# Optimization experiments

Measured on AMD Instinct MI355X. Metric: run time of the kernel, lower is better.

Reference implementation:

```python
import jax, jax.numpy as jnp
import numpy as np

B, T, D, H, L, V = 16, 1024, 512, 8, 6, 96
HS = D // H
FF = 4 * D


def setup_inputs() -> dict:
    key = jax.random.key(0)
    ks = jax.random.split(key, 16)
    n = lambda k, shape: jax.random.normal(k, shape, jnp.float32) * 0.02
    return {
        "idx": jax.random.randint(ks[0], (B, T), 0, V),
        "targets": jax.random.randint(ks[1], (B, T), 0, V),
        "tok_emb": n(ks[2], (V, D)),
        "pos_emb": n(ks[3], (T, D)),
        "Wq": n(ks[4], (L, H, D, HS)),
        "Wk": n(ks[5], (L, H, D, HS)),
        "Wv": n(ks[6], (L, H, D, HS)),
        "Wproj": n(ks[7], (L, D, D)),
        "bproj": jnp.zeros((L, D), jnp.float32),
        "W1": n(ks[8], (L, D, FF)),
        "b1": jnp.zeros((L, FF), jnp.float32),
        "W2": n(ks[9], (L, FF, D)),
        "b2": jnp.zeros((L, D), jnp.float32),
        "ln1_s": jnp.ones((L, D), jnp.float32),
        "ln1_b": jnp.zeros((L, D), jnp.float32),
        "ln2_s": jnp.ones((L, D), jnp.float32),
        "ln2_b": jnp.zeros((L, D), jnp.float32),
        "lnf_s": jnp.ones((D,), jnp.float32),
        "lnf_b": jnp.zeros((D,), jnp.float32),
        "Wout": n(ks[10], (D, V)),
        "bout": jnp.zeros((V,), jnp.float32),
    }


def _ln(x, s, b, eps=1e-5):
    m = x.mean(-1, keepdims=True)
    v = ((x - m) ** 2).mean(-1, keepdims=True)
    return (x - m) * jax.lax.rsqrt(v + eps) * s + b


def reference(idx, targets, tok_emb, pos_emb, Wq, Wk, Wv, Wproj, bproj,
              W1, b1, W2, b2, ln1_s, ln1_b, ln2_s, ln2_b, lnf_s, lnf_b,
              Wout, bout):
    x = tok_emb[idx] + pos_emb[:T]  # [B,T,D]
    causal = jnp.tril(jnp.ones((T, T), jnp.bool_))
    scale = D ** (-0.5)  # NOTE: source scales by full channel dim, not head_size
    for l in range(L):
        h = _ln(x, ln1_s[l], ln1_b[l])
        q = jnp.einsum("btd,hdk->bhtk", h, Wq[l])
        k = jnp.einsum("btd,hdk->bhtk", h, Wk[l])
        v = jnp.einsum("btd,hdk->bhtk", h, Wv[l])
        att = jnp.einsum("bhtk,bhsk->bhts", q, k) * scale
        att = jnp.where(causal, att, -jnp.inf)
        att = jax.nn.softmax(att, axis=-1)
        o = jnp.einsum("bhts,bhsk->bhtk", att, v)
        o = o.transpose(0, 2, 1, 3).reshape(B, T, D)  # concat heads
        x = x + (o @ Wproj[l] + bproj[l])
        h2 = _ln(x, ln2_s[l], ln2_b[l])
        x = x + (jnp.maximum(h2 @ W1[l] + b1[l], 0.0) @ W2[l] + b2[l])
    x = _ln(x, lnf_s, lnf_b)
    logits = (x @ Wout + bout).reshape(B * T, V)
    logp = jax.nn.log_softmax(logits, axis=-1)
    loss = -logp[jnp.arange(B * T), targets.reshape(-1)].mean()
    return logits, loss
```

## Files before the change

### kernel.cpp

```cpp
#include <hip/hip_runtime.h>

#define B_  16
#define T_  1024
#define D_  512
#define H_  8
#define L_  6
#define V_  96
#define HS_ 64
#define FF_ 2048
#define BT_ (B_*T_)

typedef __attribute__((ext_vector_type(8))) short bf16x8;
typedef __attribute__((ext_vector_type(4))) float f32x4;

typedef __attribute__((address_space(3))) unsigned int lds_u32_t;
typedef const __attribute__((address_space(1))) unsigned int glb_u32_t;

__device__ __forceinline__ void gload16(const unsigned short* g, unsigned short* l) {
  __builtin_amdgcn_global_load_lds((glb_u32_t*)g, (lds_u32_t*)l, 16, 0, 0);
}

__device__ __forceinline__ unsigned short f2b(float f) {
  unsigned u = __float_as_uint(f);
  unsigned r = (u + 0x7FFFu + ((u >> 16) & 1u)) >> 16;
  return (unsigned short)r;
}

__global__ void zero_kernel(float* p) { p[0] = 0.f; }

__global__ __launch_bounds__(128) void embed_kernel(const int* __restrict__ idx,
    const float* __restrict__ tok, const float* __restrict__ pos, float* __restrict__ x) {
  int bt = blockIdx.x;
  int t  = bt & (T_ - 1);
  int id = idx[bt];
  if (id < 0) id = 0; if (id > V_ - 1) id = V_ - 1;
  int d  = threadIdx.x * 4;
  float4 tv = *(const float4*)(tok + (size_t)id * D_ + d);
  float4 pv = *(const float4*)(pos + (size_t)t  * D_ + d);
  float4 o = {tv.x + pv.x, tv.y + pv.y, tv.z + pv.z, tv.w + pv.w};
  *(float4*)(x + (size_t)bt * D_ + d) = o;
}

__global__ __launch_bounds__(256) void transpose_cvt(const float* __restrict__ src,
    unsigned short* __restrict__ dst, int R, int C, long sstride, long dstride) {
  __shared__ float t[32][33];
  const float* s = src + (size_t)blockIdx.z * sstride;
  unsigned short* d = dst + (size_t)blockIdx.z * dstride;
  int r0 = blockIdx.y * 32, c0 = blockIdx.x * 32;
  int tr = threadIdx.x >> 5, tc = threadIdx.x & 31;
#pragma unroll
  for (int i = 0; i < 4; ++i)
    t[tr + i * 8][tc] = s[(size_t)(r0 + tr + i * 8) * C + c0 + tc];
  __syncthreads();
#pragma unroll
  for (int i = 0; i < 4; ++i)
    d[(size_t)(c0 + tr + i * 8) * R + r0 + tc] = f2b(t[tc][tr + i * 8]);
}

template<bool BF16OUT>
__global__ __launch_bounds__(256) void ln_kernel(const float* __restrict__ x,
    const float* __restrict__ s, const float* __restrict__ b, void* __restrict__ outv) {
  int wave = threadIdx.x >> 6;
  int lane = threadIdx.x & 63;
  int r = blockIdx.x * 4 + wave;
  const float* xr = x + (size_t)r * D_;
  float vals[8];
  float sum = 0.f;
#pragma unroll
  for (int j = 0; j < 8; ++j) { vals[j] = xr[j * 64 + lane]; sum += vals[j]; }
#pragma unroll
  for (int o = 32; o > 0; o >>= 1) sum += __shfl_xor(sum, o, 64);
  float mean = sum * (1.f / D_);
  float vs = 0.f;
#pragma unroll
  for (int j = 0; j < 8; ++j) { float d = vals[j] - mean; vs += d * d; }
#pragma unroll
  for (int o = 32; o > 0; o >>= 1) vs += __shfl_xor(vs, o, 64);
  float rstd = rsqrtf(vs * (1.f / D_) + 1e-5f);
#pragma unroll
  for (int j = 0; j < 8; ++j) {
    int c = j * 64 + lane;
    float v = (vals[j] - mean) * rstd * s[c] + b[c];
    if (BF16OUT) ((unsigned short*)outv)[(size_t)r * D_ + c] = f2b(v);
    else         ((float*)outv)[(size_t)r * D_ + c] = v;
  }
}

#define BK 32
template<bool ACC, bool RELU, bool BIAS, int OUTMODE>
__global__ __launch_bounds__(256) void mfma_gemm(
    const unsigned short* __restrict__ A,
    const unsigned short* __restrict__ Bt,
    const float* __restrict__ bias,
    void* __restrict__ Cv,
    int K, int ldc) {
  __shared__ unsigned short Al[128 * BK];
  __shared__ unsigned short Bl[128 * BK];
  const int m0 = blockIdx.x * 128, n0 = blockIdx.y * 128;
  const int tid = threadIdx.x;
  const int lane = tid & 63, wave = tid >> 6;
  const int wy = wave >> 1, wx = wave & 1;
  const int l15 = lane & 15, quad = lane >> 4;

  const int sbase = wave * 1024;
  const int soff  = sbase + lane * 16;
  const int r0 = soff >> 6, c0e = (soff & 63) >> 1;
  const int r1 = r0 + 64;
  const unsigned short* gA0 = A  + (size_t)(m0 + r0) * K + c0e;
  const unsigned short* gA1 = A  + (size_t)(m0 + r1) * K + c0e;
  const unsigned short* gB0 = Bt + (size_t)(n0 + r0) * K + c0e;
  const unsigned short* gB1 = Bt + (size_t)(n0 + r1) * K + c0e;
  unsigned short* lA0 = &Al[sbase >> 1];
  unsigned short* lA1 = &Al[(sbase + 4096) >> 1];
  unsigned short* lB0 = &Bl[sbase >> 1];
  unsigned short* lB1 = &Bl[(sbase + 4096) >> 1];

  f32x4 acc[4][4];
  const f32x4 z4 = {0.f, 0.f, 0.f, 0.f};
#pragma unroll
  for (int mi = 0; mi < 4; ++mi)
#pragma unroll
    for (int ni = 0; ni < 4; ++ni) acc[mi][ni] = z4;

  for (int k0 = 0; k0 < K; k0 += BK) {
    gload16(gA0 + k0, lA0);
    gload16(gA1 + k0, lA1);
    gload16(gB0 + k0, lB0);
    gload16(gB1 + k0, lB1);
    __syncthreads();
    bf16x8 af[4], bfr[4];
#pragma unroll
    for (int mi = 0; mi < 4; ++mi)
      af[mi] = *(const bf16x8*)(&Al[(wy * 64 + mi * 16 + l15) * BK + quad * 8]);
#pragma unroll
    for (int ni = 0; ni < 4; ++ni)
      bfr[ni] = *(const bf16x8*)(&Bl[(wx * 64 + ni * 16 + l15) * BK + quad * 8]);
#pragma unroll
    for (int mi = 0; mi < 4; ++mi)
#pragma unroll
      for (int ni = 0; ni < 4; ++ni)
        acc[mi][ni] = __builtin_amdgcn_mfma_f32_16x16x32_bf16(af[mi], bfr[ni], acc[mi][ni], 0, 0, 0);
    __syncthreads();
  }
#pragma unroll
  for (int mi = 0; mi < 4; ++mi) {
    int row0 = m0 + wy * 64 + mi * 16 + quad * 4;
#pragma unroll
    for (int ni = 0; ni < 4; ++ni) {
      int col = n0 + wx * 64 + ni * 16 + l15;
      float bb = BIAS ? bias[col] : 0.f;
#pragma unroll
      for (int r = 0; r < 4; ++r) {
        float v = acc[mi][ni][r] + bb;
        if (RELU) v = fmaxf(v, 0.f);
        int row = row0 + r;
        if (OUTMODE == 2) {
          int b = row >> 10, t = row & (T_ - 1);
          int h = col >> 6, hs = col & 63;
          ((unsigned short*)Cv)[((size_t)((b * H_ + h) * HS_ + hs)) * T_ + t] = f2b(v);
        } else {
          size_t off = (size_t)row * ldc + col;
          if (ACC) v += ((const float*)Cv)[off];
          if (OUTMODE == 1) ((unsigned short*)Cv)[off] = f2b(v);
          else              ((float*)Cv)[off] = v;
        }
      }
    }
  }
}

#define PSTR 72
__global__ __launch_bounds__(256) void attn_mfma(const unsigned short* __restrict__ q,
    const unsigned short* __restrict__ k, const unsigned short* __restrict__ vt,
    unsigned short* __restrict__ o) {
  __shared__ unsigned short Pbuf[2][64 * PSTR];
  __shared__ float Lsum[4][64];
  const int qt = (gridDim.x - 1) - blockIdx.x;
  const int bh = blockIdx.y;
  const int b = bh >> 3, hh = bh & 7;
  const int tid = threadIdx.x;
  const int lane = tid & 63, w = tid >> 6;
  const int l15 = lane & 15, quad = lane >> 4;
  const float CEXP = 0.044194173824159216f * 1.4426950408889634f;

  bf16x8 qf[4][2];
#pragma unroll
  for (int mi = 0; mi < 4; ++mi)
#pragma unroll
    for (int c = 0; c < 2; ++c)
      qf[mi][c] = *(const bf16x8*)(q + (size_t)(b * T_ + qt * 64 + mi * 16 + l15) * D_
                                     + hh * HS_ + c * 32 + quad * 8);

  f32x4 oacc[4];
  float psum[4][4];
  const f32x4 z4 = {0.f, 0.f, 0.f, 0.f};
#pragma unroll
  for (int mi = 0; mi < 4; ++mi) {
    oacc[mi] = z4;
#pragma unroll
    for (int r = 0; r < 4; ++r) psum[mi][r] = 0.f;
  }

  const unsigned short* kbase = k  + (size_t)(b * T_ + w * 16 + l15) * D_ + hh * HS_ + quad * 8;
  const unsigned short* vbase = vt + ((size_t)(bh * HS_ + w * 16 + l15)) * T_ + quad * 8;

  bf16x8 kf[2], vf[2];
#pragma unroll
  for (int c = 0; c < 2; ++c) {
    kf[c] = *(const bf16x8*)(kbase + c * 32);
    vf[c] = *(const bf16x8*)(vbase + c * 32);
  }

  const int gc = w * 16 + l15;

  for (int kt = 0; kt <= qt; ++kt) {
    const int ktn = (kt < qt) ? kt + 1 : qt;
    bf16x8 kfn[2], vfn[2];
#pragma unroll
    for (int c = 0; c < 2; ++c) {
      kfn[c] = *(const bf16x8*)(kbase + (size_t)ktn * 64 * D_ + c * 32);
      vfn[c] = *(const bf16x8*)(vbase + ktn * 64 + c * 32);
    }

    f32x4 s[4];
#pragma unroll
    for (int mi = 0; mi < 4; ++mi) s[mi] = z4;
    __builtin_amdgcn_s_setprio(1);
#pragma unroll
    for (int c = 0; c < 2; ++c)
#pragma unroll
      for (int mi = 0; mi < 4; ++mi)
        s[mi] = __builtin_amdgcn_mfma_f32_16x16x32_bf16(qf[mi][c], kf[c], s[mi], 0, 0, 0);
    __builtin_amdgcn_s_setprio(0);

    unsigned short* pb = Pbuf[kt & 1];
    if (kt == qt) {
#pragma unroll
      for (int mi = 0; mi < 4; ++mi)
#pragma unroll
        for (int r = 0; r < 4; ++r) {
          int row = mi * 16 + quad * 4 + r;
          float p = (gc > row) ? 0.f : exp2f(s[mi][r] * CEXP);
          unsigned short us = f2b(p);
          psum[mi][r] += __uint_as_float((unsigned)us << 16);
          pb[row * PSTR + gc] = us;
        }
    } else {
#pragma unroll
      for (int mi = 0; mi < 4; ++mi)
#pragma unroll
        for (int r = 0; r < 4; ++r) {
          int row = mi * 16 + quad * 4 + r;
          float p = exp2f(s[mi][r] * CEXP);
          unsigned short us = f2b(p);
          psum[mi][r] += __uint_as_float((unsigned)us << 16);
          pb[row * PSTR + gc] = us;
        }
    }
    __syncthreads();
    __builtin_amdgcn_s_setprio(1);
#pragma unroll
    for (int c = 0; c < 2; ++c) {
#pragma unroll
      for (int mi = 0; mi < 4; ++mi) {
        bf16x8 pf = *(const bf16x8*)(&pb[(mi * 16 + l15) * PSTR + c * 32 + quad * 8]);
        oacc[mi] = __builtin_amdgcn_mfma_f32_16x16x32_bf16(pf, vf[c], oacc[mi], 0, 0, 0);
      }
    }
    __builtin_amdgcn_s_setprio(0);
#pragma unroll
    for (int c = 0; c < 2; ++c) { kf[c] = kfn[c]; vf[c] = vfn[c]; }
  }

#pragma unroll
  for (int mi = 0; mi < 4; ++mi)
#pragma unroll
    for (int r = 0; r < 4; ++r) {
#pragma unroll
      for (int off = 1; off < 16; off <<= 1)
        psum[mi][r] += __shfl_xor(psum[mi][r], off, 64);
    }
  if (l15 == 0) {
#pragma unroll
    for (int mi = 0; mi < 4; ++mi)
#pragma unroll
      for (int r = 0; r < 4; ++r)
        Lsum[w][mi * 16 + quad * 4 + r] = psum[mi][r];
  }
  __syncthreads();
#pragma unroll
  for (int mi = 0; mi < 4; ++mi)
#pragma unroll
    for (int r = 0; r < 4; ++r) {
      int row = mi * 16 + quad * 4 + r;
      float inv = 1.f / (Lsum[0][row] + Lsum[1][row] + Lsum[2][row] + Lsum[3][row]);
      o[(size_t)(b * T_ + qt * 64 + row) * D_ + hh * HS_ + w * 16 + l15] =
          f2b(oacc[mi][r] * inv);
    }
}

__global__ __launch_bounds__(256) void gemm_f32_kernel(const float* __restrict__ A, int lda,
    const float* __restrict__ Bw, int ldb, const float* __restrict__ bias,
    float* __restrict__ C, int ldc, int K, int N) {
  __shared__ float As[16][64];
  __shared__ float Bs[16][64];
  int n0 = blockIdx.y * 64;
  int nv = N - n0; if (nv > 64) nv = 64;
  int m0 = blockIdx.x * 64;
  const int tid = threadIdx.x;
  const int tx = tid & 15, ty = tid >> 4;
  const int amm = tid >> 2;
  const int akk = (tid & 3) * 4;
  const int bkk = tid >> 4;
  const int bnn = (tid & 15) * 4;
  float acc[4][4] = {};
  for (int k0 = 0; k0 < K; k0 += 16) {
    float4 av = *(const float4*)(A + (size_t)(m0 + amm) * lda + k0 + akk);
    As[akk + 0][amm] = av.x; As[akk + 1][amm] = av.y;
    As[akk + 2][amm] = av.z; As[akk + 3][amm] = av.w;
    if (bnn < nv) {
      float4 bv = *(const float4*)(Bw + (size_t)(k0 + bkk) * ldb + n0 + bnn);
      Bs[bkk][bnn + 0] = bv.x; Bs[bkk][bnn + 1] = bv.y;
      Bs[bkk][bnn + 2] = bv.z; Bs[bkk][bnn + 3] = bv.w;
    } else {
      Bs[bkk][bnn + 0] = 0.f; Bs[bkk][bnn + 1] = 0.f;
      Bs[bkk][bnn + 2] = 0.f; Bs[bkk][bnn + 3] = 0.f;
    }
    __syncthreads();
#pragma unroll
    for (int kk = 0; kk < 16; ++kk) {
      float4 a4 = *(const float4*)(&As[kk][ty * 4]);
      float4 b4 = *(const float4*)(&Bs[kk][tx * 4]);
      float aa[4] = {a4.x, a4.y, a4.z, a4.w};
      float bb[4] = {b4.x, b4.y, b4.z, b4.w};
#pragma unroll
      for (int i = 0; i < 4; ++i)
#pragma unroll
        for (int j = 0; j < 4; ++j)
          acc[i][j] = fmaf(aa[i], bb[j], acc[i][j]);
    }
    __syncthreads();
  }
  if (tx * 4 < nv) {
#pragma unroll
    for (int i = 0; i < 4; ++i) {
      float* cp = C + (size_t)(m0 + ty * 4 + i) * ldc + n0 + tx * 4;
      float4 st = {acc[i][0] + bias[n0 + tx * 4 + 0], acc[i][1] + bias[n0 + tx * 4 + 1],
                   acc[i][2] + bias[n0 + tx * 4 + 2], acc[i][3] + bias[n0 + tx * 4 + 3]};
      *(float4*)cp = st;
    }
  }
}

__global__ __launch_bounds__(256) void loss_kernel(const float* __restrict__ logits,
    const int* __restrict__ targets, float* __restrict__ loss_acc) {
  __shared__ float wsum[4];
  int wave = threadIdx.x >> 6, lane = threadIdx.x & 63;
  float local = 0.f;
  for (int r = blockIdx.x * 4 + wave; r < BT_; r += gridDim.x * 4) {
    const float* lr = logits + (size_t)r * V_;
    float v0 = lr[lane];
    float v1 = (lane < 32) ? lr[64 + lane] : -INFINITY;
    float mx = fmaxf(v0, v1);
#pragma unroll
    for (int o = 32; o > 0; o >>= 1) mx = fmaxf(mx, __shfl_xor(mx, o, 64));
    float se = expf(v0 - mx) + ((lane < 32) ? expf(v1 - mx) : 0.f);
#pragma unroll
    for (int o = 32; o > 0; o >>= 1) se += __shfl_xor(se, o, 64);
    if (lane == 0) {
      int tg = targets[r];
      if (tg < 0) tg = 0; if (tg > V_ - 1) tg = V_ - 1;
      local += (mx + logf(se)) - lr[tg];
    }
  }
  if (lane == 0) wsum[wave] = local;
  __syncthreads();
  if (threadIdx.x == 0)
    atomicAdd(loss_acc, wsum[0] + wsum[1] + wsum[2] + wsum[3]);
}

__global__ void loss_finalize_kernel(const float* __restrict__ acc, float* __restrict__ out) {
  out[(size_t)BT_ * V_] = acc[0] * (1.f / BT_);
}

static void* g_ws_fallback = nullptr;

extern "C" void kernel_launch(void* const* d_in, const int* in_sizes, int n_in,
                              void* d_out, int out_size, void* d_ws, size_t ws_size,
                              hipStream_t stream) {
  const int*   idx     = (const int*)d_in[0];
  const int*   targets = (const int*)d_in[1];
  const float* tok  = (const float*)d_in[2];
  const float* pos  = (const float*)d_in[3];
  const float* Wq   = (const float*)d_in[4];
  const float* Wk   = (const float*)d_in[5];
  const float* Wv   = (const float*)d_in[6];
  const float* Wp   = (const float*)d_in[7];
  const float* bp   = (const float*)d_in[8];
  const float* W1   = (const float*)d_in[9];
  const float* b1   = (const float*)d_in[10];
  const float* W2   = (const float*)d_in[11];
  const float* b2   = (const float*)d_in[12];
  const float* l1s  = (const float*)d_in[13];
  const float* l1b  = (const float*)d_in[14];
  const float* l2s  = (const float*)d_in[15];
  const float* l2b  = (const float*)d_in[16];
  const float* lfs  = (const float*)d_in[17];
  const float* lfb  = (const float*)d_in[18];
  const float* Wout = (const float*)d_in[19];
  const float* bout = (const float*)d_in[20];
  float* out = (float*)d_out;

  const size_t n_x  = (size_t)BT_ * D_;
  const size_t n_wT = 9437184;
  const size_t need_floats = n_x + n_x + n_x / 2 + n_x / 2 + n_x / 2 +
                             (size_t)BT_ * FF_ / 2 + n_wT + 256;
  const size_t need_bytes  = need_floats * sizeof(float);

  float* ws;
  if (ws_size >= need_bytes) {
    ws = (float*)d_ws;
  } else {
    if (!g_ws_fallback) (void)hipMalloc(&g_ws_fallback, need_bytes);
    ws = (float*)g_ws_fallback;
  }

  size_t off = 0;
  float* x  = ws + off; off += n_x;
  float* qf32 = ws + off; off += n_x;
  unsigned short* qb = (unsigned short*)qf32;
  unsigned short* kb  = (unsigned short*)(ws + off); off += n_x / 2;
  unsigned short* vtb = (unsigned short*)(ws + off); off += n_x / 2;
  unsigned short* hb  = (unsigned short*)(ws + off); off += n_x / 2;
  unsigned short* ffb = (unsigned short*)(ws + off); off += (size_t)BT_ * FF_ / 2;
  unsigned short* wqT = (unsigned short*)(ws + off);
  unsigned short* wkT = wqT + (size_t)L_ * D_ * D_;
  unsigned short* wvT = wkT + (size_t)L_ * D_ * D_;
  unsigned short* wpT = wvT + (size_t)L_ * D_ * D_;
  unsigned short* w1T = wpT + (size_t)L_ * D_ * D_;
  unsigned short* w2T = w1T + (size_t)L_ * D_ * FF_;
  off += n_wT;
  float* lacc = ws + off;

  zero_kernel<<<1, 1, 0, stream>>>(lacc);
  embed_kernel<<<BT_, 128, 0, stream>>>(idx, tok, pos, x);

  transpose_cvt<<<dim3(2, 16, 48), 256, 0, stream>>>(Wq, wqT, 512, 64, 32768, 32768);
  transpose_cvt<<<dim3(2, 16, 48), 256, 0, stream>>>(Wk, wkT, 512, 64, 32768, 32768);
  transpose_cvt<<<dim3(2, 16, 48), 256, 0, stream>>>(Wv, wvT, 512, 64, 32768, 32768);
  transpose_cvt<<<dim3(16, 16, 6), 256, 0, stream>>>(Wp, wpT, 512, 512, 262144, 262144);
  transpose_cvt<<<dim3(64, 16, 6), 256, 0, stream>>>(W1, w1T, 512, 2048, 1048576, 1048576);
  transpose_cvt<<<dim3(16, 64, 6), 256, 0, stream>>>(W2, w2T, 2048, 512, 1048576, 1048576);

  const dim3 gD(BT_ / 128, D_ / 128);
  const dim3 gF(BT_ / 128, FF_ / 128);

  for (int l = 0; l < L_; ++l) {
    ln_kernel<true><<<BT_ / 4, 256, 0, stream>>>(x, l1s + (size_t)l * D_, l1b + (size_t)l * D_, hb);
    mfma_gemm<false, false, false, 1><<<gD, 256, 0, stream>>>(
        hb, wqT + (size_t)l * D_ * D_, nullptr, qb, D_, D_);
    mfma_gemm<false, false, false, 1><<<gD, 256, 0, stream>>>(
        hb, wkT + (size_t)l * D_ * D_, nullptr, kb, D_, D_);
    mfma_gemm<false, false, false, 2><<<gD, 256, 0, stream>>>(
        hb, wvT + (size_t)l * D_ * D_, nullptr, vtb, D_, D_);
    attn_mfma<<<dim3(T_ / 64, B_ * H_), 256, 0, stream>>>(qb, kb, vtb, hb);
    mfma_gemm<true, false, true, 0><<<gD, 256, 0, stream>>>(
        hb, wpT + (size_t)l * D_ * D_, bp + (size_t)l * D_, x, D_, D_);
    ln_kernel<true><<<BT_ / 4, 256, 0, stream>>>(x, l2s + (size_t)l * D_, l2b + (size_t)l * D_, hb);
    mfma_gemm<false, true, true, 1><<<gF, 256, 0, stream>>>(
        hb, w1T + (size_t)l * D_ * FF_, b1 + (size_t)l * FF_, ffb, D_, FF_);
    mfma_gemm<true, false, true, 0><<<gD, 256, 0, stream>>>(
        ffb, w2T + (size_t)l * FF_ * D_, b2 + (size_t)l * D_, x, FF_, D_);
  }

  ln_kernel<false><<<BT_ / 4, 256, 0, stream>>>(x, lfs, lfb, qf32);
  gemm_f32_kernel<<<dim3(BT_ / 64, 2), 256, 0, stream>>>(
      qf32, D_, Wout, V_, bout, out, V_, D_, V_);
  loss_kernel<<<64, 256, 0, stream>>>(out, targets, lacc);
  loss_finalize_kernel<<<1, 1, 0, stream>>>(lacc, out);
}
```

Baseline: 2.136 ms.

## Fuse QKV projections into one GEMM and double-buffer GEMM LDS tiles

Concatenates the transposed Wq/Wk/Wv weights per layer so a single GEMM with 12 column tiles writes Q and K into an interleaved row-major buffer of stride 1024 and V into the transposed layout. Attention is updated to read Q/K with the new stride. Separately, the MFMA GEMM now double-buffers its LDS tiles, issuing the next K-step's global-to-LDS loads before computing the current one and using one barrier per step instead of two. This aims to cut launch count, re-reads of the normalized activations, and load stalls, at the cost of twice the LDS per block, which may lower occupancy.

Measured after the change: 2.065 ms. 1.03x faster.

```diff
diff --git a/kernel.cpp b/kernel.cpp
--- a/kernel.cpp
+++ b/kernel.cpp
@@ -9,6 +9,7 @@
 #define HS_ 64
 #define FF_ 2048
 #define BT_ (B_*T_)
+#define QKS 1024
 
 typedef __attribute__((ext_vector_type(8))) short bf16x8;
 typedef __attribute__((ext_vector_type(4))) float f32x4;
@@ -42,10 +43,12 @@
 }
 
 __global__ __launch_bounds__(256) void transpose_cvt(const float* __restrict__ src,
-    unsigned short* __restrict__ dst, int R, int C, long sstride, long dstride) {
+    unsigned short* __restrict__ dst, int R, int C, long sstride, long dstride,
+    int zper, long zouter) {
   __shared__ float t[32][33];
   const float* s = src + (size_t)blockIdx.z * sstride;
-  unsigned short* d = dst + (size_t)blockIdx.z * dstride;
+  unsigned short* d = dst + (size_t)(blockIdx.z / zper) * zouter
+                          + (size_t)(blockIdx.z % zper) * dstride;
   int r0 = blockIdx.y * 32, c0 = blockIdx.x * 32;
   int tr = threadIdx.x >> 5, tc = threadIdx.x & 31;
 #pragma unroll
@@ -92,10 +95,10 @@
     const unsigned short* __restrict__ A,
     const unsigned short* __restrict__ Bt,
     const float* __restrict__ bias,
-    void* __restrict__ Cv,
+    void* __restrict__ Cv, void* __restrict__ Cv2,
     int K, int ldc) {
-  __shared__ unsigned short Al[128 * BK];
-  __shared__ unsigned short Bl[128 * BK];
+  __shared__ unsigned short Al[2][128 * BK];
+  __shared__ unsigned short Bl[2][128 * BK];
   const int m0 = blockIdx.x * 128, n0 = blockIdx.y * 128;
   const int tid = threadIdx.x;
   const int lane = tid & 63, wave = tid >> 6;
@@ -106,14 +109,11 @@
   const int soff  = sbase + lane * 16;
   const int r0 = soff >> 6, c0e = (soff & 63) >> 1;
   const int r1 = r0 + 64;
+  const int ls = sbase >> 1;
   const unsigned short* gA0 = A  + (size_t)(m0 + r0) * K + c0e;
   const unsigned short* gA1 = A  + (size_t)(m0 + r1) * K + c0e;
   const unsigned short* gB0 = Bt + (size_t)(n0 + r0) * K + c0e;
   const unsigned short* gB1 = Bt + (size_t)(n0 + r1) * K + c0e;
-  unsigned short* lA0 = &Al[sbase >> 1];
-  unsigned short* lA1 = &Al[(sbase + 4096) >> 1];
-  unsigned short* lB0 = &Bl[sbase >> 1];
-  unsigned short* lB1 = &Bl[(sbase + 4096) >> 1];
 
   f32x4 acc[4][4];
   const f32x4 z4 = {0.f, 0.f, 0.f, 0.f};
@@ -122,26 +122,40 @@
 #pragma unroll
     for (int ni = 0; ni < 4; ++ni) acc[mi][ni] = z4;
 
-  for (int k0 = 0; k0 < K; k0 += BK) {
-    gload16(gA0 + k0, lA0);
-    gload16(gA1 + k0, lA1);
-    gload16(gB0 + k0, lB0);
-    gload16(gB1 + k0, lB1);
-    __syncthreads();
+  gload16(gA0, &Al[0][ls]);
+  gload16(gA1, &Al[0][ls + 2048]);
+  gload16(gB0, &Bl[0][ls]);
+  gload16(gB1, &Bl[0][ls + 2048]);
+  __syncthreads();
+
+  const int nsteps = K / BK;
+  int cur = 0;
+  for (int s = 0; s < nsteps; ++s) {
+    if (s + 1 < nsteps) {
+      const int k0 = (s + 1) * BK;
+      gload16(gA0 + k0, &Al[cur ^ 1][ls]);
+      gload16(gA1 + k0, &Al[cur ^ 1][ls + 2048]);
+      gload16(gB0 + k0, &Bl[cur ^ 1][ls]);
+      gload16(gB1 + k0, &Bl[cur ^ 1][ls + 2048]);
+    }
     bf16x8 af[4], bfr[4];
 #pragma unroll
     for (int mi = 0; mi < 4; ++mi)
-      af[mi] = *(const bf16x8*)(&Al[(wy * 64 + mi * 16 + l15) * BK + quad * 8]);
+      af[mi] = *(const bf16x8*)(&Al[cur][(wy * 64 + mi * 16 + l15) * BK + quad * 8]);
 #pragma unroll
     for (int ni = 0; ni < 4; ++ni)
-      bfr[ni] = *(const bf16x8*)(&Bl[(wx * 64 + ni * 16 + l15) * BK + quad * 8]);
+      bfr[ni] = *(const bf16x8*)(&Bl[cur][(wx * 64 + ni * 16 + l15) * BK + quad * 8]);
 #pragma unroll
     for (int mi = 0; mi < 4; ++mi)
 #pragma unroll
       for (int ni = 0; ni < 4; ++ni)
         acc[mi][ni] = __builtin_amdgcn_mfma_f32_16x16x32_bf16(af[mi], bfr[ni], acc[mi][ni], 0, 0, 0);
-    __syncthreads();
-  }
+    if (s + 1 < nsteps) {
+      __syncthreads();
+      cur ^= 1;
+    }
+  }
+
 #pragma unroll
   for (int mi = 0; mi < 4; ++mi) {
     int row0 = m0 + wy * 64 + mi * 16 + quad * 4;
@@ -154,10 +168,15 @@
         float v = acc[mi][ni][r] + bb;
         if (RELU) v = fmaxf(v, 0.f);
         int row = row0 + r;
-        if (OUTMODE == 2) {
-          int b = row >> 10, t = row & (T_ - 1);
-          int h = col >> 6, hs = col & 63;
-          ((unsigned short*)Cv)[((size_t)((b * H_ + h) * HS_ + hs)) * T_ + t] = f2b(v);
+        if (OUTMODE == 3) {
+          if (col < 1024) {
+            ((unsigned short*)Cv)[(size_t)row * QKS + col] = f2b(v);
+          } else {
+            int vcol = col - 1024;
+            int b = row >> 10, t = row & (T_ - 1);
+            int h = vcol >> 6, hs = vcol & 63;
+            ((unsigned short*)Cv2)[((size_t)((b * H_ + h) * HS_ + hs)) * T_ + t] = f2b(v);
+          }
         } else {
           size_t off = (size_t)row * ldc + col;
           if (ACC) v += ((const float*)Cv)[off];
@@ -188,7 +207,7 @@
   for (int mi = 0; mi < 4; ++mi)
 #pragma unroll
     for (int c = 0; c < 2; ++c)
-      qf[mi][c] = *(const bf16x8*)(q + (size_t)(b * T_ + qt * 64 + mi * 16 + l15) * D_
+      qf[mi][c] = *(const bf16x8*)(q + (size_t)(b * T_ + qt * 64 + mi * 16 + l15) * QKS
                                      + hh * HS_ + c * 32 + quad * 8);
 
   f32x4 oacc[4];
@@ -201,7 +220,7 @@
     for (int r = 0; r < 4; ++r) psum[mi][r] = 0.f;
   }
 
-  const unsigned short* kbase = k  + (size_t)(b * T_ + w * 16 + l15) * D_ + hh * HS_ + quad * 8;
+  const unsigned short* kbase = k  + (size_t)(b * T_ + w * 16 + l15) * QKS + hh * HS_ + quad * 8;
   const unsigned short* vbase = vt + ((size_t)(bh * HS_ + w * 16 + l15)) * T_ + quad * 8;
 
   bf16x8 kf[2], vf[2];
@@ -218,7 +237,7 @@
     bf16x8 kfn[2], vfn[2];
 #pragma unroll
     for (int c = 0; c < 2; ++c) {
-      kfn[c] = *(const bf16x8*)(kbase + (size_t)ktn * 64 * D_ + c * 32);
+      kfn[c] = *(const bf16x8*)(kbase + (size_t)ktn * 64 * QKS + c * 32);
       vfn[c] = *(const bf16x8*)(vbase + ktn * 64 + c * 32);
     }
 
@@ -428,49 +447,48 @@
   size_t off = 0;
   float* x  = ws + off; off += n_x;
   float* qf32 = ws + off; off += n_x;
-  unsigned short* qb = (unsigned short*)qf32;
-  unsigned short* kb  = (unsigned short*)(ws + off); off += n_x / 2;
+  unsigned short* qkb = (unsigned short*)qf32;
+  unsigned short* spare = (unsigned short*)(ws + off); off += n_x / 2;
   unsigned short* vtb = (unsigned short*)(ws + off); off += n_x / 2;
   unsigned short* hb  = (unsigned short*)(ws + off); off += n_x / 2;
   unsigned short* ffb = (unsigned short*)(ws + off); off += (size_t)BT_ * FF_ / 2;
-  unsigned short* wqT = (unsigned short*)(ws + off);
-  unsigned short* wkT = wqT + (size_t)L_ * D_ * D_;
-  unsigned short* wvT = wkT + (size_t)L_ * D_ * D_;
-  unsigned short* wpT = wvT + (size_t)L_ * D_ * D_;
+  unsigned short* wqkvT = (unsigned short*)(ws + off);
+  unsigned short* wpT = wqkvT + (size_t)L_ * 3 * D_ * D_;
   unsigned short* w1T = wpT + (size_t)L_ * D_ * D_;
   unsigned short* w2T = w1T + (size_t)L_ * D_ * FF_;
   off += n_wT;
   float* lacc = ws + off;
+  (void)spare;
+
+  const long DD = (long)D_ * D_;
+  const long L3DD = 3 * DD;
 
   zero_kernel<<<1, 1, 0, stream>>>(lacc);
   embed_kernel<<<BT_, 128, 0, stream>>>(idx, tok, pos, x);
 
-  transpose_cvt<<<dim3(2, 16, 48), 256, 0, stream>>>(Wq, wqT, 512, 64, 32768, 32768);
-  transpose_cvt<<<dim3(2, 16, 48), 256, 0, stream>>>(Wk, wkT, 512, 64, 32768, 32768);
-  transpose_cvt<<<dim3(2, 16, 48), 256, 0, stream>>>(Wv, wvT, 512, 64, 32768, 32768);
-  transpose_cvt<<<dim3(16, 16, 6), 256, 0, stream>>>(Wp, wpT, 512, 512, 262144, 262144);
-  transpose_cvt<<<dim3(64, 16, 6), 256, 0, stream>>>(W1, w1T, 512, 2048, 1048576, 1048576);
-  transpose_cvt<<<dim3(16, 64, 6), 256, 0, stream>>>(W2, w2T, 2048, 512, 1048576, 1048576);
-
+  transpose_cvt<<<dim3(2, 16, 48), 256, 0, stream>>>(Wq, wqkvT,            512, 64, 32768, 32768, 8, L3DD);
+  transpose_cvt<<<dim3(2, 16, 48), 256, 0, stream>>>(Wk, wqkvT + DD,       512, 64, 32768, 32768, 8, L3DD);
+  transpose_cvt<<<dim3(2, 16, 48), 256, 0, stream>>>(Wv, wqkvT + 2 * DD,   512, 64, 32768, 32768, 8, L3DD);
+  transpose_cvt<<<dim3(16, 16, 6), 256, 0, stream>>>(Wp, wpT, 512, 512, 262144, 0, 1, 262144);
+  transpose_cvt<<<dim3(64, 16, 6), 256, 0, stream>>>(W1, w1T, 512, 2048, 1048576, 0, 1, 1048576);
+  transpose_cvt<<<dim3(16, 64, 6), 256, 0, stream>>>(W2, w2T, 2048, 512, 1048576, 0, 1, 1048576);
+
+  const dim3 gQKV(BT_ / 128, 12);
   const dim3 gD(BT_ / 128, D_ / 128);
   const dim3 gF(BT_ / 128, FF_ / 128);
 
   for (int l = 0; l < L_; ++l) {
     ln_kernel<true><<<BT_ / 4, 256, 0, stream>>>(x, l1s + (size_t)l * D_, l1b + (size_t)l * D_, hb);
-    mfma_gemm<false, false, false, 1><<<gD, 256, 0, stream>>>(
-        hb, wqT + (size_t)l * D_ * D_, nullptr, qb, D_, D_);
-    mfma_gemm<false, false, false, 1><<<gD, 256, 0, stream>>>(
-        hb, wkT + (size_t)l * D_ * D_, nullptr, kb, D_, D_);
-    mfma_gemm<false, false, false, 2><<<gD, 256, 0, stream>>>(
-        hb, wvT + (size_t)l * D_ * D_, nullptr, vtb, D_, D_);
-    attn_mfma<<<dim3(T_ / 64, B_ * H_), 256, 0, stream>>>(qb, kb, vtb, hb);
+    mfma_gemm<false, false, false, 3><<<gQKV, 256, 0, stream>>>(
+        hb, wqkvT + (size_t)l * L3DD, nullptr, qkb, vtb, D_, 0);
+    attn_mfma<<<dim3(T_ / 64, B_ * H_), 256, 0, stream>>>(qkb, qkb + 512, vtb, hb);
     mfma_gemm<true, false, true, 0><<<gD, 256, 0, stream>>>(
-        hb, wpT + (size_t)l * D_ * D_, bp + (size_t)l * D_, x, D_, D_);
+        hb, wpT + (size_t)l * DD, bp + (size_t)l * D_, x, nullptr, D_, D_);
     ln_kernel<true><<<BT_ / 4, 256, 0, stream>>>(x, l2s + (size_t)l * D_, l2b + (size_t)l * D_, hb);
     mfma_gemm<false, true, true, 1><<<gF, 256, 0, stream>>>(
-        hb, w1T + (size_t)l * D_ * FF_, b1 + (size_t)l * FF_, ffb, D_, FF_);
+        hb, w1T + (size_t)l * D_ * FF_, b1 + (size_t)l * FF_, ffb, nullptr, D_, FF_);
     mfma_gemm<true, false, true, 0><<<gD, 256, 0, stream>>>(
-        ffb, w2T + (size_t)l * FF_ * D_, b2 + (size_t)l * D_, x, FF_, D_);
+        ffb, w2T + (size_t)l * FF_ * D_, b2 + (size_t)l * D_, x, nullptr, FF_, D_);
   }
 
   ln_kernel<false><<<BT_ / 4, 256, 0, stream>>>(x, lfs, lfb, qf32);
```
